# Optimization experiments

Measured on AMD Instinct MI355X. Metric: run time of the kernel, lower is better.

Reference implementation:

```python
import jax, jax.numpy as jnp
import numpy as np

NUM_GROUPS = 2048  # ix values drawn from [0, NUM_GROUPS); stands in for torch.unique's group count

def setup_inputs() -> dict:
    key = jax.random.key(0)
    ks = jax.random.split(key, 9)
    B, E, D = 2, 32768, 512
    s = 1.0 / np.sqrt(D)  # nn.Linear default init scale
    x = jax.random.normal(ks[0], (B, E, D), jnp.float32)
    ix = jax.random.randint(ks[1], (E,), 0, NUM_GROUPS)
    Wf = jax.random.uniform(ks[2], (D, D), jnp.float32, -s, s)
    bf = jax.random.uniform(ks[3], (D,), jnp.float32, -s, s)
    Wg = jax.random.uniform(ks[4], (D, D), jnp.float32, -s, s)
    bg = jax.random.uniform(ks[5], (D,), jnp.float32, -s, s)
    Wh = jax.random.uniform(ks[6], (D, D), jnp.float32, -s, s)
    bh = jax.random.uniform(ks[7], (D,), jnp.float32, -s, s)
    return {"x": x, "ix": ix, "Wf": Wf, "bf": bf, "Wg": Wg, "bg": bg, "Wh": Wh, "bh": bh}

def reference(x, ix, Wf, bf, Wg, bg, Wh, bh):
    # Linear projections (nn.Linear: x @ W.T + b)
    logits = jnp.einsum('bed,kd->bek', x, Wg) + bg  # g(x): (B,E,D)
    vals   = jnp.einsum('bed,kd->bek', x, Wf) + bf  # f(x): (B,E,D)
    # Move edges to leading axis for segment ops: (E,B,D)
    lt = jnp.transpose(logits, (1, 0, 2))
    vt = jnp.transpose(vals, (1, 0, 2))
    # Group-wise (scatter) softmax over edges sharing the same ix
    m = jax.ops.segment_max(lt, ix, num_segments=NUM_GROUPS)      # (G,B,D)
    e = jnp.exp(lt - m[ix])                                        # (E,B,D)
    denom = jax.ops.segment_sum(e, ix, num_segments=NUM_GROUPS)   # (G,B,D)
    w = e / denom[ix]                                              # (E,B,D)
    # Weighted scatter-sum per group
    y = jax.ops.segment_sum(vt * w, ix, num_segments=NUM_GROUPS)  # (G,B,D)
    y = jnp.transpose(y, (1, 0, 2))                                # (B,G,D)
    out = jnp.einsum('bgd,kd->bgk', y, Wh) + bh                    # h(y)
    return out[:, ix]                                              # expand back to (B,E,D)
```

## Files before the change

### kernel.cpp

```cpp
#include <hip/hip_runtime.h>
#include <hip/hip_bf16.h>
#include <cstdint>
#include <cstddef>

typedef __bf16 bf16x8 __attribute__((ext_vector_type(8)));
typedef float f32x4 __attribute__((ext_vector_type(4)));
using u16 = unsigned short;

#define NUM_GROUPS_C 2048

__device__ __forceinline__ u16 f2bf(float f) {
  union { float f; uint32_t u; } c; c.f = f;
  uint32_t r = (c.u + 0x7fffu + ((c.u >> 16) & 1u)) >> 16;
  return (u16)r;
}
__device__ __forceinline__ float bf2f(u16 h) {
  union { uint32_t u; float f; } c; c.u = ((uint32_t)h) << 16; return c.f;
}

__device__ __forceinline__ void glds16(const u16* g, void* l) {
  __builtin_amdgcn_global_load_lds((const __attribute__((address_space(1))) void*)g,
                                   (__attribute__((address_space(3))) void*)l, 16, 0, 0);
}

__global__ void cast_f32_bf16(const float* __restrict__ src, u16* __restrict__ dst, long n4) {
  long i = (long)blockIdx.x * blockDim.x + threadIdx.x;
  long stride = (long)gridDim.x * blockDim.x;
  for (; i < n4; i += stride) {
    float4 v = reinterpret_cast<const float4*>(src)[i];
    uint2 o;
    o.x = (uint32_t)f2bf(v.x) | ((uint32_t)f2bf(v.y) << 16);
    o.y = (uint32_t)f2bf(v.z) | ((uint32_t)f2bf(v.w) << 16);
    reinterpret_cast<uint2*>(dst)[i] = o;
  }
}

__global__ void cast_w3(const float* __restrict__ w0, const float* __restrict__ w1,
                        const float* __restrict__ w2,
                        u16* __restrict__ o0, u16* __restrict__ o1, u16* __restrict__ o2,
                        int n4) {
  const float* src = (blockIdx.y == 0) ? w0 : (blockIdx.y == 1) ? w1 : w2;
  u16* dst = (blockIdx.y == 0) ? o0 : (blockIdx.y == 1) ? o1 : o2;
  int i = blockIdx.x * blockDim.x + threadIdx.x;
  int stride = gridDim.x * blockDim.x;
  for (; i < n4; i += stride) {
    float4 v = reinterpret_cast<const float4*>(src)[i];
    uint2 o;
    o.x = (uint32_t)f2bf(v.x) | ((uint32_t)f2bf(v.y) << 16);
    o.y = (uint32_t)f2bf(v.z) | ((uint32_t)f2bf(v.w) << 16);
    reinterpret_cast<uint2*>(dst)[i] = o;
  }
}

__global__ void zero_i32(int* p, int n) {
  int i = blockIdx.x * blockDim.x + threadIdx.x;
  if (i < n) p[i] = 0;
}
__global__ void count_k(const int* __restrict__ ix, int* __restrict__ cnt, int E) {
  int e = blockIdx.x * blockDim.x + threadIdx.x;
  if (e < E) atomicAdd(&cnt[ix[e]], 1);
}
__global__ void scan_k(const int* __restrict__ cnt, int* __restrict__ offs,
                       int* __restrict__ cursor, int G) {
  __shared__ int part[256];
  int t = threadIdx.x;
  int gpt = G / 256;
  int base = t * gpt;
  int loc[8];
  int s = 0;
  for (int j = 0; j < gpt; ++j) { loc[j] = cnt[base + j]; s += loc[j]; }
  part[t] = s;
  __syncthreads();
  for (int off = 1; off < 256; off <<= 1) {
    int v = (t >= off) ? part[t - off] : 0;
    __syncthreads();
    part[t] += v;
    __syncthreads();
  }
  int run = part[t] - s;
  for (int j = 0; j < gpt; ++j) {
    offs[base + j] = run;
    cursor[base + j] = run;
    run += loc[j];
  }
}
__global__ void scatter_k(const int* __restrict__ ix, int* __restrict__ cursor,
                          int* __restrict__ elist, int E) {
  int e = blockIdx.x * blockDim.x + threadIdx.x;
  if (e < E) {
    int g = ix[e];
    int pos = atomicAdd(&cursor[g], 1);
    elist[pos] = e;
  }
}

__global__ __launch_bounds__(512, 2)
void gemm256_fg8(const u16* __restrict__ A,
                 const u16* __restrict__ B0g, const u16* __restrict__ B1g,
                 const float* __restrict__ bias0, const float* __restrict__ bias1,
                 u16* __restrict__ C0, u16* __restrict__ C1,
                 int K, int N) {
  __shared__ u16 lds[65536];

  const int tid  = threadIdx.x;
  const int lane = tid & 63;
  const int wid  = tid >> 6;
  const int wm   = wid >> 2;
  const int wn   = wid & 3;
  const int fr   = lane & 15;
  const int fq   = lane >> 4;
  const int swr  = fr & 7;

  const int nwg = gridDim.x, cpx = nwg >> 3, wg = blockIdx.x;
  const int swz = (wg & 7) * cpx + (wg >> 3);
  const int mt = swz >> 2, ns = swz & 3;
  const u16* Bm     = (ns < 2) ? B0g : B1g;
  const float* bias = (ns < 2) ? bias0 : bias1;
  u16* C            = (ns < 2) ? C0 : C1;
  const int n0 = (ns & 1) * 256, m0 = mt * 256;

  const int r8   = tid >> 3;
  const int scol = ((tid & 7) ^ (r8 & 7)) << 3;
  const u16* Ab = A  + (size_t)m0 * K + scol;
  const u16* Bb = Bm + (size_t)n0 * K + scol;
  char* ldsb = (char*)lds;

  auto stage_ht = [&](int p, int isB, int h, int kt) {
    const u16* src = (isB ? Bb : Ab) + (size_t)(h * 128 + r8) * K + kt * 64;
    char* dst = ldsb + p * 65536 + isB * 32768 + h * 16384 + wid * 1024;
    glds16(src, dst);
    glds16(src + (size_t)64 * K, dst + 8192);
  };

#define RD_A(dst, mi_, kk_) \
  dst = *(const bf16x8*)(sA_ + (((mi_) * 32 + wm * 16 + fr) << 7) + (((((kk_) << 2) | fq) ^ swr) << 4))
#define RD_B(dst, nj_, kk_) \
  dst = *(const bf16x8*)(sB_ + (((nj_) * 64 + wn * 16 + fr) << 7) + (((((kk_) << 2) | fq) ^ swr) << 4))
#define MFMA_Q(accm, accn, af, bf_)                                                \
  __builtin_amdgcn_s_setprio(1);                                                  \
  _Pragma("unroll") for (int j = 0; j < 4; ++j)                                    \
  _Pragma("unroll") for (int jn = 0; jn < 2; ++jn)                                 \
  _Pragma("unroll") for (int kk = 0; kk < 2; ++kk)                                 \
    acc[(accm) + j][(accn) + jn] = __builtin_amdgcn_mfma_f32_16x16x32_bf16(        \
        af[j][kk], bf_[jn][kk], acc[(accm) + j][(accn) + jn], 0, 0, 0);            \
  __builtin_amdgcn_s_setprio(0);

  f32x4 acc[8][4] = {};
  const int NT = K >> 6;

  stage_ht(0, 1, 0, 0);
  stage_ht(0, 0, 0, 0);
  stage_ht(0, 1, 1, 0);
  stage_ht(0, 0, 1, 0);
  asm volatile("s_waitcnt vmcnt(4)" ::: "memory");
  __builtin_amdgcn_s_barrier();

  for (int kt = 0; kt < NT; ++kt) {
    const int cb = kt & 1, nb = cb ^ 1;
    const int ks = (kt + 1 < NT) ? kt + 1 : NT - 1;
    const char* sA_ = ldsb + cb * 65536;
    const char* sB_ = sA_ + 32768;
    bf16x8 a0[4][2], a1[4][2], b0[2][2], b1[2][2];

    #pragma unroll
    for (int j = 0; j < 4; ++j) { RD_A(a0[j][0], j, 0); RD_A(a0[j][1], j, 1); }
    #pragma unroll
    for (int j = 0; j < 2; ++j) { RD_B(b0[j][0], j, 0); RD_B(b0[j][1], j, 1); }
    stage_ht(nb, 1, 0, ks);
    asm volatile("s_waitcnt vmcnt(4)" ::: "memory");
    __builtin_amdgcn_s_barrier();
    MFMA_Q(0, 0, a0, b0)
    __builtin_amdgcn_s_barrier();

    #pragma unroll
    for (int j = 0; j < 2; ++j) { RD_B(b1[j][0], j + 2, 0); RD_B(b1[j][1], j + 2, 1); }
    stage_ht(nb, 0, 0, ks);
    asm volatile("s_waitcnt vmcnt(4)" ::: "memory");
    __builtin_amdgcn_s_barrier();
    MFMA_Q(0, 2, a0, b1)
    __builtin_amdgcn_s_barrier();

    #pragma unroll
    for (int j = 0; j < 4; ++j) { RD_A(a1[j][0], j + 4, 0); RD_A(a1[j][1], j + 4, 1); }
    stage_ht(nb, 1, 1, ks);
    asm volatile("s_waitcnt vmcnt(4)" ::: "memory");
    __builtin_amdgcn_s_barrier();
    MFMA_Q(4, 2, a1, b1)
    __builtin_amdgcn_s_barrier();

    stage_ht(nb, 0, 1, ks);
    asm volatile("s_waitcnt vmcnt(4)" ::: "memory");
    __builtin_amdgcn_s_barrier();
    MFMA_Q(4, 0, a1, b0)
    __builtin_amdgcn_s_barrier();
  }
  asm volatile("s_waitcnt vmcnt(0)" ::: "memory");

  #pragma unroll
  for (int mi = 0; mi < 8; ++mi) {
    const int row = m0 + mi * 32 + wm * 16 + fq * 4;
    #pragma unroll
    for (int ni = 0; ni < 4; ++ni) {
      const int col = n0 + ni * 64 + wn * 16 + fr;
      const float bvv = bias[col];
      #pragma unroll
      for (int r = 0; r < 4; ++r)
        C[(size_t)(row + r) * N + col] = f2bf(acc[mi][ni][r] + bvv);
    }
  }
#undef RD_A
#undef RD_B
#undef MFMA_Q
}

__device__ __forceinline__ void stage_tile_128x64(const u16* __restrict__ src, int ld,
                                                  u16* lds, int tid) {
  int wid = tid >> 6;
  #pragma unroll
  for (int i = 0; i < 4; ++i) {
    int c = i * 256 + tid;
    const u16* g = src + (size_t)(c >> 3) * ld + ((c & 7) << 3);
    char* l = (char*)lds + ((i * 4 + wid) << 10);
    glds16(g, l);
  }
}

__global__ __launch_bounds__(256)
void gemm_bf16_nt_f32out(const u16* __restrict__ A, const u16* __restrict__ Bm,
                         const float* __restrict__ bias,
                         float* __restrict__ C, int K, int N) {
  __shared__ u16 sA[128 * 64];
  __shared__ u16 sB[128 * 64];

  int tid = threadIdx.x;
  const int m0 = blockIdx.x * 128, n0 = blockIdx.y * 128;
  const u16* Ap = A + (size_t)m0 * K;
  const u16* Bp = Bm + (size_t)n0 * K;

  int lane = tid & 63;
  int wid = tid >> 6;
  int wm = wid >> 1, wn = wid & 1;
  int fr = lane & 15;
  int fq = lane >> 4;

  f32x4 acc[4][4] = {};

  for (int k0 = 0; k0 < K; k0 += 64) {
    stage_tile_128x64(Ap + k0, K, sA, tid);
    stage_tile_128x64(Bp + k0, K, sB, tid);
    __syncthreads();
    #pragma unroll
    for (int kk = 0; kk < 2; ++kk) {
      bf16x8 af[4], bfrag[4];
      #pragma unroll
      for (int mi = 0; mi < 4; ++mi)
        af[mi] = *reinterpret_cast<const bf16x8*>(&sA[(wm * 64 + mi * 16 + fr) * 64 + kk * 32 + fq * 8]);
      #pragma unroll
      for (int nj = 0; nj < 4; ++nj)
        bfrag[nj] = *reinterpret_cast<const bf16x8*>(&sB[(wn * 64 + nj * 16 + fr) * 64 + kk * 32 + fq * 8]);
      #pragma unroll
      for (int mi = 0; mi < 4; ++mi)
        #pragma unroll
        for (int nj = 0; nj < 4; ++nj)
          acc[mi][nj] = __builtin_amdgcn_mfma_f32_16x16x32_bf16(af[mi], bfrag[nj], acc[mi][nj], 0, 0, 0);
    }
    __syncthreads();
  }

  #pragma unroll
  for (int nj = 0; nj < 4; ++nj) {
    int col = n0 + wn * 64 + nj * 16 + fr;
    float bv = bias[col];
    #pragma unroll
    for (int mi = 0; mi < 4; ++mi) {
      int rowb = m0 + wm * 64 + mi * 16 + fq * 4;
      #pragma unroll
      for (int r = 0; r < 4; ++r)
        C[(size_t)(rowb + r) * N + col] = acc[mi][nj][r] + bv;
    }
  }
}

__global__ __launch_bounds__(256)
void seg_softmax(const u16* __restrict__ lg, const u16* __restrict__ vl,
                 const int* __restrict__ cnt, const int* __restrict__ offs,
                 const int* __restrict__ elist,
                 u16* __restrict__ y, int E, int D, int B, int G) {
  __shared__ int eids[256];
  int g = blockIdx.x / B;
  int b = blockIdx.x - g * B;
  int t = threadIdx.x;
  int n = cnt[g], start = offs[g];
  int d0 = t * 2;

  float m0 = -1e30f, m1 = -1e30f, s0 = 0.f, s1 = 0.f, a0 = 0.f, a1 = 0.f;
  for (int c0 = 0; c0 < n; c0 += 256) {
    int nc = n - c0; if (nc > 256) nc = 256;
    __syncthreads();
    if (t < nc) eids[t] = elist[start + c0 + t];
    __syncthreads();
    for (int i = 0; i < nc; ++i) {
      size_t base = ((size_t)b * E + eids[i]) * D + d0;
      uint32_t lu = *reinterpret_cast<const uint32_t*>(lg + base);
      uint32_t vu = *reinterpret_cast<const uint32_t*>(vl + base);
      float l0 = bf2f((u16)(lu & 0xffffu)), l1 = bf2f((u16)(lu >> 16));
      float v0 = bf2f((u16)(vu & 0xffffu)), v1 = bf2f((u16)(vu >> 16));
      float nm0 = fmaxf(m0, l0);
      float sc0 = __expf(m0 - nm0), w0 = __expf(l0 - nm0);
      s0 = s0 * sc0 + w0; a0 = a0 * sc0 + w0 * v0; m0 = nm0;
      float nm1 = fmaxf(m1, l1);
      float sc1 = __expf(m1 - nm1), w1 = __expf(l1 - nm1);
      s1 = s1 * sc1 + w1; a1 = a1 * sc1 + w1 * v1; m1 = nm1;
    }
  }
  float r0 = (n > 0) ? a0 / s0 : 0.f;
  float r1 = (n > 0) ? a1 / s1 : 0.f;
  size_t yoff = ((size_t)b * G + g) * D + d0;
  uint32_t o = (uint32_t)f2bf(r0) | ((uint32_t)f2bf(r1) << 16);
  *reinterpret_cast<uint32_t*>(y + yoff) = o;
}

__global__ __launch_bounds__(256)
void gather_k(const float* __restrict__ of, const int* __restrict__ ix,
              float* __restrict__ out, int E, int D, int G, int B) {
  const int rsub = threadIdx.x >> 7;
  const int t = threadIdx.x & 127;
  const long nrows = (long)B * E;
  for (long row = (long)blockIdx.x * 2 + rsub; row < nrows; row += (long)gridDim.x * 2) {
    int b = (int)(row / E);
    int e = (int)(row - (long)b * E);
    int g = ix[e];
    const float4* src = reinterpret_cast<const float4*>(of + ((size_t)b * G + g) * D);
    float4* dst = reinterpret_cast<float4*>(out + (size_t)row * D);
    dst[t] = src[t];
  }
}

extern "C" void kernel_launch(void* const* d_in, const int* in_sizes, int n_in,
                              void* d_out, int out_size, void* d_ws, size_t ws_size,
                              hipStream_t stream) {
  const float* x   = (const float*)d_in[0];
  const int*   ix  = (const int*)d_in[1];
  const float* Wf  = (const float*)d_in[2];
  const float* bfb = (const float*)d_in[3];
  const float* Wg  = (const float*)d_in[4];
  const float* bg  = (const float*)d_in[5];
  const float* Wh  = (const float*)d_in[6];
  const float* bh  = (const float*)d_in[7];

  const int E = in_sizes[1];
  const int D = in_sizes[3];
  const int B = in_sizes[0] / (E * D);
  const int G = NUM_GROUPS_C;
  const int M = B * E;
  const long xn = (long)M * D;

  char* ws = (char*)d_ws;
  size_t off = 0;
  auto alloc = [&](size_t bytes) -> char* {
    char* p = ws + off;
    off += (bytes + 255) & ~(size_t)255;
    return p;
  };
  u16* xb  = (u16*)alloc((size_t)M * D * 2);
  u16* lgb = (u16*)alloc((size_t)M * D * 2);
  u16* vlb = (u16*)alloc((size_t)M * D * 2);
  u16* Wgb = (u16*)alloc((size_t)D * D * 2);
  u16* Wfb = (u16*)alloc((size_t)D * D * 2);
  u16* Whb = (u16*)alloc((size_t)D * D * 2);
  u16* yb  = (u16*)alloc((size_t)B * G * D * 2);
  float* ofb = (float*)alloc((size_t)B * G * D * 4);
  int* cnt    = (int*)alloc((size_t)G * 4);
  int* offs   = (int*)alloc((size_t)G * 4);
  int* cursor = (int*)alloc((size_t)G * 4);
  int* elist  = (int*)alloc((size_t)E * 4);

  cast_f32_bf16<<<2048, 256, 0, stream>>>(x, xb, xn / 4);
  dim3 gw(64, 3);
  cast_w3<<<gw, 256, 0, stream>>>(Wg, Wf, Wh, Wgb, Wfb, Whb, D * D / 4);

  zero_i32<<<(G + 255) / 256, 256, 0, stream>>>(cnt, G);
  count_k<<<(E + 255) / 256, 256, 0, stream>>>(ix, cnt, E);
  scan_k<<<1, 256, 0, stream>>>(cnt, offs, cursor, G);
  scatter_k<<<(E + 255) / 256, 256, 0, stream>>>(ix, cursor, elist, E);

  gemm256_fg8<<<(M / 256) * 4, 512, 0, stream>>>(xb, Wgb, Wfb, bg, bfb, lgb, vlb, D, D);

  seg_softmax<<<G * B, 256, 0, stream>>>(lgb, vlb, cnt, offs, elist, yb, E, D, B, G);

  dim3 gh((B * G) / 128, D / 128);
  gemm_bf16_nt_f32out<<<gh, 256, 0, stream>>>(yb, Whb, bh, ofb, D, D);

  gather_k<<<2048, 256, 0, stream>>>(ofb, ix, (float*)d_out, E, D, G, B);
}
```

Baseline: 223.8 us.

## Split 256x256 projection GEMM tile across 16 waves instead of 8

The fused f/g projection GEMM now launches 1024-thread blocks (16 waves) per 256x256 tile instead of 512. Each wave computes half as many output fragments (4x4 accumulators instead of 8x4), and each thread issues one LDS staging load per half-tile instead of two, with the wait counts adjusted to match. The aim is more latency hiding and less register pressure per wave. In exchange, occupancy drops to one block per CU and there are more waves taking part in each barrier.

```diff
diff --git a/kernel.cpp b/kernel.cpp
--- a/kernel.cpp
+++ b/kernel.cpp
@@ -94,8 +94,8 @@
   }
 }
 
-__global__ __launch_bounds__(512, 2)
-void gemm256_fg8(const u16* __restrict__ A,
+__global__ __launch_bounds__(1024, 1)
+void gemm256_w16(const u16* __restrict__ A,
                  const u16* __restrict__ B0g, const u16* __restrict__ B1g,
                  const float* __restrict__ bias0, const float* __restrict__ bias1,
                  u16* __restrict__ C0, u16* __restrict__ C1,
@@ -129,30 +129,35 @@
     const u16* src = (isB ? Bb : Ab) + (size_t)(h * 128 + r8) * K + kt * 64;
     char* dst = ldsb + p * 65536 + isB * 32768 + h * 16384 + wid * 1024;
     glds16(src, dst);
-    glds16(src + (size_t)64 * K, dst + 8192);
   };
 
-#define RD_A(dst, mi_, kk_) \
-  dst = *(const bf16x8*)(sA_ + (((mi_) * 32 + wm * 16 + fr) << 7) + (((((kk_) << 2) | fq) ^ swr) << 4))
-#define RD_B(dst, nj_, kk_) \
-  dst = *(const bf16x8*)(sB_ + (((nj_) * 64 + wn * 16 + fr) << 7) + (((((kk_) << 2) | fq) ^ swr) << 4))
-#define MFMA_Q(accm, accn, af, bf_)                                                \
+#define RD2_A(dst, mio)                                                             \
+  _Pragma("unroll") for (int j = 0; j < 2; ++j)                                     \
+  _Pragma("unroll") for (int kk = 0; kk < 2; ++kk)                                  \
+    dst[j][kk] = *(const bf16x8*)(sA_ + ((((mio) + j) * 64 + wm * 16 + fr) << 7)    \
+                                       + ((((kk << 2) | fq) ^ swr) << 4));
+#define RD2_B(dst, njo)                                                             \
+  _Pragma("unroll") for (int j = 0; j < 2; ++j)                                     \
+  _Pragma("unroll") for (int kk = 0; kk < 2; ++kk)                                  \
+    dst[j][kk] = *(const bf16x8*)(sB_ + ((((njo) + j) * 64 + wn * 16 + fr) << 7)    \
+                                       + ((((kk << 2) | fq) ^ swr) << 4));
+#define MFMA_Q(qm_, qn_, af, bf_)                                                  \
   __builtin_amdgcn_s_setprio(1);                                                  \
-  _Pragma("unroll") for (int j = 0; j < 4; ++j)                                    \
+  _Pragma("unroll") for (int j = 0; j < 2; ++j)                                    \
   _Pragma("unroll") for (int jn = 0; jn < 2; ++jn)                                 \
   _Pragma("unroll") for (int kk = 0; kk < 2; ++kk)                                 \
-    acc[(accm) + j][(accn) + jn] = __builtin_amdgcn_mfma_f32_16x16x32_bf16(        \
-        af[j][kk], bf_[jn][kk], acc[(accm) + j][(accn) + jn], 0, 0, 0);            \
+    acc[(qm_) * 2 + j][(qn_) * 2 + jn] = __builtin_amdgcn_mfma_f32_16x16x32_bf16(  \
+        af[j][kk], bf_[jn][kk], acc[(qm_) * 2 + j][(qn_) * 2 + jn], 0, 0, 0);      \
   __builtin_amdgcn_s_setprio(0);
 
-  f32x4 acc[8][4] = {};
+  f32x4 acc[4][4] = {};
   const int NT = K >> 6;
 
   stage_ht(0, 1, 0, 0);
   stage_ht(0, 0, 0, 0);
   stage_ht(0, 1, 1, 0);
   stage_ht(0, 0, 1, 0);
-  asm volatile("s_waitcnt vmcnt(4)" ::: "memory");
+  asm volatile("s_waitcnt vmcnt(2)" ::: "memory");
   __builtin_amdgcn_s_barrier();
 
   for (int kt = 0; kt < NT; ++kt) {
@@ -160,45 +165,41 @@
     const int ks = (kt + 1 < NT) ? kt + 1 : NT - 1;
     const char* sA_ = ldsb + cb * 65536;
     const char* sB_ = sA_ + 32768;
-    bf16x8 a0[4][2], a1[4][2], b0[2][2], b1[2][2];
-
-    #pragma unroll
-    for (int j = 0; j < 4; ++j) { RD_A(a0[j][0], j, 0); RD_A(a0[j][1], j, 1); }
-    #pragma unroll
-    for (int j = 0; j < 2; ++j) { RD_B(b0[j][0], j, 0); RD_B(b0[j][1], j, 1); }
+    bf16x8 a0[2][2], a1[2][2], b0[2][2], b1[2][2];
+
+    RD2_A(a0, 0)
+    RD2_B(b0, 0)
     stage_ht(nb, 1, 0, ks);
-    asm volatile("s_waitcnt vmcnt(4)" ::: "memory");
+    asm volatile("s_waitcnt vmcnt(2)" ::: "memory");
     __builtin_amdgcn_s_barrier();
     MFMA_Q(0, 0, a0, b0)
     __builtin_amdgcn_s_barrier();
 
-    #pragma unroll
-    for (int j = 0; j < 2; ++j) { RD_B(b1[j][0], j + 2, 0); RD_B(b1[j][1], j + 2, 1); }
+    RD2_B(b1, 2)
     stage_ht(nb, 0, 0, ks);
-    asm volatile("s_waitcnt vmcnt(4)" ::: "memory");
-    __builtin_amdgcn_s_barrier();
-    MFMA_Q(0, 2, a0, b1)
-    __builtin_amdgcn_s_barrier();
-
-    #pragma unroll
-    for (int j = 0; j < 4; ++j) { RD_A(a1[j][0], j + 4, 0); RD_A(a1[j][1], j + 4, 1); }
+    asm volatile("s_waitcnt vmcnt(2)" ::: "memory");
+    __builtin_amdgcn_s_barrier();
+    MFMA_Q(0, 1, a0, b1)
+    __builtin_amdgcn_s_barrier();
+
+    RD2_A(a1, 2)
     stage_ht(nb, 1, 1, ks);
-    asm volatile("s_waitcnt vmcnt(4)" ::: "memory");
-    __builtin_amdgcn_s_barrier();
-    MFMA_Q(4, 2, a1, b1)
+    asm volatile("s_waitcnt vmcnt(2)" ::: "memory");
+    __builtin_amdgcn_s_barrier();
+    MFMA_Q(1, 1, a1, b1)
     __builtin_amdgcn_s_barrier();
 
     stage_ht(nb, 0, 1, ks);
-    asm volatile("s_waitcnt vmcnt(4)" ::: "memory");
-    __builtin_amdgcn_s_barrier();
-    MFMA_Q(4, 0, a1, b0)
+    asm volatile("s_waitcnt vmcnt(2)" ::: "memory");
+    __builtin_amdgcn_s_barrier();
+    MFMA_Q(1, 0, a1, b0)
     __builtin_amdgcn_s_barrier();
   }
   asm volatile("s_waitcnt vmcnt(0)" ::: "memory");
 
   #pragma unroll
-  for (int mi = 0; mi < 8; ++mi) {
-    const int row = m0 + mi * 32 + wm * 16 + fq * 4;
+  for (int mi = 0; mi < 4; ++mi) {
+    const int row = m0 + mi * 64 + wm * 16 + fq * 4;
     #pragma unroll
     for (int ni = 0; ni < 4; ++ni) {
       const int col = n0 + ni * 64 + wn * 16 + fr;
@@ -208,8 +209,8 @@
         C[(size_t)(row + r) * N + col] = f2bf(acc[mi][ni][r] + bvv);
     }
   }
-#undef RD_A
-#undef RD_B
+#undef RD2_A
+#undef RD2_B
 #undef MFMA_Q
 }
 
@@ -384,7 +385,7 @@
   scan_k<<<1, 256, 0, stream>>>(cnt, offs, cursor, G);
   scatter_k<<<(E + 255) / 256, 256, 0, stream>>>(ix, cursor, elist, E);
 
-  gemm256_fg8<<<(M / 256) * 4, 512, 0, stream>>>(xb, Wgb, Wfb, bg, bfb, lgb, vlb, D, D);
+  gemm256_w16<<<(M / 256) * 4, 1024, 0, stream>>>(xb, Wgb, Wfb, bg, bfb, lgb, vlb, D, D);
 
   seg_softmax<<<G * B, 256, 0, stream>>>(lgb, vlb, cnt, offs, elist, yb, E, D, B, G);
 
```

After: 257.0 us. 14.8% more time.
